# Optimization experiments

Hardware: AMD Instinct MI355X
Metric: run time of the kernel (lower is better)

## Reference

```python
import jax, jax.numpy as jnp
import numpy as np

B, L, C, H, DK, MAXREL = 4, 1024, 768, 12, 64, 7
NEG = -2.0 ** 15  # masked_fill value


def _rel_pos_table(L, m):
    # abs distance, compressed logarithmically beyond m, clipped to [0, 2m]
    i = jnp.arange(L, dtype=jnp.float32)
    d = jnp.abs(i[:, None] - i[None, :])
    comp = m + jnp.log2(jnp.maximum(d - m, 1.0))
    d = jnp.where(d > m, comp, d)
    return jnp.clip(d, 0, 2 * m).astype(jnp.int32)  # [L, L]


def setup_inputs() -> dict:
    key = jax.random.key(0)
    ks = jax.random.split(key, 16)
    s = 0.02
    return {
        "qx": jax.random.normal(ks[0], (B, L, C), jnp.float32),
        "kx": jax.random.normal(ks[1], (B, L, C), jnp.float32),
        "vx": jax.random.normal(ks[2], (B, L, C), jnp.float32),
        "WQ_w": jax.random.normal(ks[3], (C, H * DK), jnp.float32) * s,
        "WQ_b": jnp.zeros((H * DK,), jnp.float32),
        "WK_w": jax.random.normal(ks[4], (C, H * DK), jnp.float32) * s,
        "WK_b": jnp.zeros((H * DK,), jnp.float32),
        "WV_w": jax.random.normal(ks[5], (C, H * DK), jnp.float32) * s,
        "WV_b": jnp.zeros((H * DK,), jnp.float32),
        "WO_w": jax.random.normal(ks[6], (H * DK, C), jnp.float32) * s,
        "WO_b": jnp.zeros((C,), jnp.float32),
        "embK": jax.random.normal(ks[7], (2 * MAXREL + 1, H), jnp.float32),
        "embB": jax.random.normal(ks[8], (2 * MAXREL + 1, H), jnp.float32) * s,
        "preScores": jax.random.normal(ks[9], (B, H, L, L), jnp.float32) * 0.1,
        "maskPAD": jnp.ones((B, L, L), jnp.int32),
    }


def reference(qx, kx, vx, WQ_w, WQ_b, WK_w, WK_b, WV_w, WV_b, WO_w, WO_b,
              embK, embB, preScores, maskPAD):
    q = (qx @ WQ_w + WQ_b).reshape(B, L, H, DK).transpose(0, 2, 1, 3)  # [B,H,L,dk]
    k = (kx @ WK_w + WK_b).reshape(B, L, H, DK).transpose(0, 2, 1, 3)
    v = (vx @ WV_w + WV_b).reshape(B, L, H, DK).transpose(0, 2, 1, 3)

    scores = jnp.einsum('bhid,bhjd->bhij', q, k) / np.sqrt(DK).astype(np.float32)

    tab = _rel_pos_table(L, MAXREL)                 # [L, L] int
    relK = jnp.transpose(embK[tab], (2, 1, 0))      # [H, L, L] (torch transpose(0,-1))
    relB = jnp.transpose(embB[tab], (2, 1, 0))
    scores = scores * relK[None] + relB[None]

    scores = scores + preScores
    scores = jnp.where((maskPAD == 0)[:, None, :, :], jnp.float32(NEG), scores)

    alpha = jax.nn.softmax(scores, axis=-1)         # dropout is identity in eval
    z = jnp.einsum('bhij,bhjd->bhid', alpha, v)     # [B,H,L,dk]
    z = z.transpose(0, 2, 1, 3).reshape(B, L, H * DK)
    z = z @ WO_w + WO_b
    return (z, scores)
```

## Files before the change

kernel.cpp:

```cpp
#include <hip/hip_runtime.h>
#include <stdint.h>


typedef __attribute__((ext_vector_type(4))) float f32x4;
typedef __attribute__((ext_vector_type(4))) int   i32x4;
typedef __attribute__((ext_vector_type(8))) short short8;
typedef __attribute__((ext_vector_type(4))) unsigned int u32x4;
typedef __attribute__((ext_vector_type(2))) unsigned int u32x2;

__device__ __forceinline__ unsigned short f2bf(float f) {
  unsigned int u = __float_as_uint(f);
  u += 0x7fffu + ((u >> 16) & 1u);
  return (unsigned short)(u >> 16);
}

__global__ __launch_bounds__(256) void conv_x_kernel(
    const float* __restrict__ qx, const float* __restrict__ kx,
    const float* __restrict__ vx, unsigned short* __restrict__ out) {
  int v = blockIdx.x * 256 + threadIdx.x;
  int mat = v / 786432;
  int r = v - mat * 786432;
  const float* src = (mat == 0) ? qx : (mat == 1) ? kx : vx;
  f32x4 x = ((const f32x4*)src)[r];
  union { unsigned short s[4]; u32x2 u; } o;
  o.s[0] = f2bf(x[0]); o.s[1] = f2bf(x[1]); o.s[2] = f2bf(x[2]); o.s[3] = f2bf(x[3]);
  ((u32x2*)out)[v] = o.u;
}

__global__ __launch_bounds__(256) void conv_w_kernel(
    const float* __restrict__ w0, const float* __restrict__ w1,
    const float* __restrict__ w2, const float* __restrict__ w3,
    unsigned short* __restrict__ out) {
  __shared__ float T[64][65];
  int bx = blockIdx.x;
  int mat = bx / 144; int t2 = bx - mat * 144;
  int kt = t2 / 12, nt = t2 - kt * 12;
  int k0 = kt * 64, n0 = nt * 64;
  const float* W = (mat == 0) ? w0 : (mat == 1) ? w1 : (mat == 2) ? w2 : w3;
  unsigned short* WT = out + (size_t)mat * 589824;
  int t = threadIdx.x;
  int lr = t >> 4;
  int lc = (t & 15) * 4;
#pragma unroll
  for (int p = 0; p < 4; p++) {
    int row = p * 16 + lr;
    f32x4 x = *(const f32x4*)&W[(size_t)(k0 + row) * 768 + n0 + lc];
    T[lc + 0][row] = x[0]; T[lc + 1][row] = x[1];
    T[lc + 2][row] = x[2]; T[lc + 3][row] = x[3];
  }
  __syncthreads();
#pragma unroll
  for (int p = 0; p < 4; p++) {
    int row = p * 16 + lr;
    union { unsigned short s[4]; u32x2 u; } o;
    o.s[0] = f2bf(T[row][lc + 0]); o.s[1] = f2bf(T[row][lc + 1]);
    o.s[2] = f2bf(T[row][lc + 2]); o.s[3] = f2bf(T[row][lc + 3]);
    *(u32x2*)&WT[(size_t)(n0 + row) * 768 + k0 + lc] = o.u;
  }
}

__global__ __launch_bounds__(256, 2) void qkv_gemm_kernel(
    const unsigned short* __restrict__ xbf, const unsigned short* __restrict__ wt,
    const float* __restrict__ bq, const float* __restrict__ bk, const float* __restrict__ bv,
    unsigned short* __restrict__ qo, unsigned short* __restrict__ ko,
    unsigned short* __restrict__ vto) {
  __shared__ unsigned short SM[2][2][128 * 72];
  int bx = blockIdx.x;
  int mat = bx / 192; int rem = bx - mat * 192;
  int mt = rem / 6, nt = rem - mt * 6;
  int m0 = mt * 128, n0 = nt * 128;
  const unsigned short* A = xbf + (size_t)mat * 4096 * 768;
  const unsigned short* Bm = wt + (size_t)mat * 768 * 768;
  int t = threadIdx.x;
  int wave = t >> 6, lane = t & 63;
  int wm = (wave >> 1) * 64, wn = (wave & 1) * 64;
  int col = lane & 15, quad = lane >> 4;
  int srow = t >> 3;
  int sch = (t & 7) * 8;

  f32x4 acc[4][4];
#pragma unroll
  for (int i = 0; i < 4; i++)
#pragma unroll
    for (int j = 0; j < 4; j++) acc[i][j] = (f32x4){0.f, 0.f, 0.f, 0.f};

  u32x4 ra[4], rb[4];
#pragma unroll
  for (int p = 0; p < 4; p++) {
    ra[p] = *(const u32x4*)&A[(size_t)(m0 + srow + p * 32) * 768 + sch];
    rb[p] = *(const u32x4*)&Bm[(size_t)(n0 + srow + p * 32) * 768 + sch];
  }
#pragma unroll
  for (int p = 0; p < 4; p++) {
    *(u32x4*)&SM[0][0][(srow + p * 32) * 72 + sch] = ra[p];
    *(u32x4*)&SM[0][1][(srow + p * 32) * 72 + sch] = rb[p];
  }
#pragma unroll
  for (int p = 0; p < 4; p++) {
    ra[p] = *(const u32x4*)&A[(size_t)(m0 + srow + p * 32) * 768 + 64 + sch];
    rb[p] = *(const u32x4*)&Bm[(size_t)(n0 + srow + p * 32) * 768 + 64 + sch];
  }
  __syncthreads();

  for (int it = 0; it < 12; ++it) {
    const unsigned short* As = SM[it & 1][0];
    const unsigned short* Bs = SM[it & 1][1];
#pragma unroll
    for (int c = 0; c < 2; c++) {
      short8 af[4], bf[4];
#pragma unroll
      for (int i = 0; i < 4; i++) {
        af[i] = *(const short8*)&As[(wm + i * 16 + col) * 72 + c * 32 + quad * 8];
        bf[i] = *(const short8*)&Bs[(wn + i * 16 + col) * 72 + c * 32 + quad * 8];
      }
#pragma unroll
      for (int i = 0; i < 4; i++)
#pragma unroll
        for (int j = 0; j < 4; j++)
          acc[i][j] = __builtin_amdgcn_mfma_f32_16x16x32_bf16(af[i], bf[j], acc[i][j], 0, 0, 0);
    }
    if (it < 11) {
      unsigned short* An = SM[(it + 1) & 1][0];
      unsigned short* Bn = SM[(it + 1) & 1][1];
#pragma unroll
      for (int p = 0; p < 4; p++) {
        *(u32x4*)&An[(srow + p * 32) * 72 + sch] = ra[p];
        *(u32x4*)&Bn[(srow + p * 32) * 72 + sch] = rb[p];
      }
      if (it < 10) {
        int kk2 = (it + 2) * 64;
#pragma unroll
        for (int p = 0; p < 4; p++) {
          ra[p] = *(const u32x4*)&A[(size_t)(m0 + srow + p * 32) * 768 + kk2 + sch];
          rb[p] = *(const u32x4*)&Bm[(size_t)(n0 + srow + p * 32) * 768 + kk2 + sch];
        }
      }
      __syncthreads();
    }
  }

  if (mat != 2) {
    const float* bias = (mat == 0) ? bq : bk;
    unsigned short* dst = (mat == 0) ? qo : ko;
#pragma unroll
    for (int j = 0; j < 4; j++) {
      int gn = n0 + wn + j * 16 + col;
      float bsv = bias[gn];
      int h = gn >> 6, d = gn & 63;
#pragma unroll
      for (int i = 0; i < 4; i++) {
#pragma unroll
        for (int r = 0; r < 4; r++) {
          int gm = m0 + wm + i * 16 + quad * 4 + r;
          int b = gm >> 10, l = gm & 1023;
          dst[((size_t)(b * 12 + h) * 1024 + l) * 64 + d] = f2bf(acc[i][j][r] + bsv);
        }
      }
    }
  } else {
    unsigned short* Tr = &SM[0][0][0];
    __syncthreads();
#pragma unroll
    for (int j = 0; j < 4; j++) {
      int n = wn + j * 16 + col;
      float bsv = bv[n0 + n];
#pragma unroll
      for (int i = 0; i < 4; i++) {
        int m = wm + i * 16 + quad * 4;
        union { unsigned short s[4]; u32x2 u; } pk;
#pragma unroll
        for (int r = 0; r < 4; r++) pk.s[r] = f2bf(acc[i][j][r] + bsv);
        *(u32x2*)&Tr[(size_t)n * 132 + m] = pk.u;
      }
    }
    __syncthreads();
#pragma unroll
    for (int p = 0; p < 8; p++) {
      int row = (t >> 4) + p * 16;
      int ch = (t & 15) * 8;
      u32x4 val = *(const u32x4*)&Tr[(size_t)row * 132 + ch];
      int gn = n0 + row;
      int h = gn >> 6, d = gn & 63;
      int gm = m0 + ch;
      int b = gm >> 10, l = gm & 1023;
      *(u32x4*)&vto[((size_t)(b * 12 + h) * 64 + d) * 1024 + l] = val;
    }
  }
}

struct KV { u32x4 k0, k1, v0, v1; };

__device__ __forceinline__ void attn_body(
    int j0, int j2, bool stageNext, bool pf2,
    const unsigned short* KsC, const unsigned short* VsC,
    unsigned short* KsN, unsigned short* VsN,
    f32x4* preC, i32x4* mkC, KV& kvW, KV& kvF,
    const short8* qf, f32x4* oacc, float& m_s, float& l_s,
    const unsigned short* kbase, const unsigned short* vbase,
    const float* pbase, const int* mbase, float* sbase,
    unsigned short* Ps, const float* eK, const float* eB,
    int lrow, int gi, int srow, int sch, int col, int quad, int wave) {
  if (pf2) {
    kvF.k0 = *(const u32x4*)&kbase[(size_t)(j2 + srow) * 64 + sch];
    kvF.k1 = *(const u32x4*)&kbase[(size_t)(j2 + srow + 32) * 64 + sch];
    kvF.v0 = *(const u32x4*)&vbase[(size_t)srow * 1024 + j2 + sch];
    kvF.v1 = *(const u32x4*)&vbase[(size_t)(srow + 32) * 1024 + j2 + sch];
  }
  f32x4 sacc[4];
#pragma unroll
  for (int ns = 0; ns < 4; ns++) sacc[ns] = (f32x4){0.f, 0.f, 0.f, 0.f};
#pragma unroll
  for (int c = 0; c < 2; c++) {
#pragma unroll
    for (int ns = 0; ns < 4; ns++) {
      short8 kf = *(const short8*)&KsC[(ns * 16 + col) * 72 + c * 32 + quad * 8];
      sacc[ns] = __builtin_amdgcn_mfma_f32_16x16x32_bf16(kf, qf[c], sacc[ns], 0, 0, 0);
    }
  }
  float sv[4][4];
#pragma unroll
  for (int ns = 0; ns < 4; ns++) {
    int gj0 = j0 + ns * 16 + quad * 4;
    f32x4 sout;
#pragma unroll
    for (int r = 0; r < 4; r++) {
      int dd = gi - (gj0 + r); dd = dd < 0 ? -dd : dd;
      int idx;
      if (dd <= 7) idx = dd;
      else { idx = 38 - __clz(dd - 7); idx = idx > 14 ? 14 : idx; }
      float s = sacc[ns][r] * 0.125f * eK[idx] + eB[idx] + preC[ns][r];
      if (mkC[ns][r] == 0) s = -32768.0f;
      sout[r] = s; sv[ns][r] = s;
    }
    *(f32x4*)&sbase[(size_t)lrow * 1024 + gj0] = sout;
  }
  if (pf2) {
#pragma unroll
    for (int ns = 0; ns < 4; ns++) {
      preC[ns] = *(const f32x4*)&pbase[(size_t)lrow * 1024 + j2 + ns * 16 + quad * 4];
      mkC[ns] = *(const i32x4*)&mbase[(size_t)lrow * 1024 + j2 + ns * 16 + quad * 4];
    }
  }
  float mx = sv[0][0];
#pragma unroll
  for (int ns = 0; ns < 4; ns++)
#pragma unroll
    for (int r = 0; r < 4; r++) mx = fmaxf(mx, sv[ns][r]);
  mx = fmaxf(mx, __shfl_xor(mx, 16));
  mx = fmaxf(mx, __shfl_xor(mx, 32));
  float mn = fmaxf(m_s, mx);
  float alpha = __expf(m_s - mn);
  float rs = 0.f;
#pragma unroll
  for (int ns = 0; ns < 4; ns++)
#pragma unroll
    for (int r = 0; r < 4; r++) { float p = __expf(sv[ns][r] - mn); sv[ns][r] = p; rs += p; }
  rs += __shfl_xor(rs, 16); rs += __shfl_xor(rs, 32);
  l_s = l_s * alpha + rs;
  m_s = mn;
#pragma unroll
  for (int nd = 0; nd < 4; nd++)
#pragma unroll
    for (int r = 0; r < 4; r++) oacc[nd][r] *= alpha;
#pragma unroll
  for (int ns = 0; ns < 4; ns++) {
    union { unsigned short s[4]; u32x2 u; } pk;
#pragma unroll
    for (int r = 0; r < 4; r++) pk.s[r] = f2bf(sv[ns][r]);
    *(u32x2*)&Ps[(size_t)lrow * 72 + ns * 16 + quad * 4] = pk.u;
  }
#pragma unroll
  for (int c2 = 0; c2 < 2; c2++) {
    short8 pf = *(const short8*)&Ps[(wave * 16 + col) * 72 + c2 * 32 + quad * 8];
#pragma unroll
    for (int nd = 0; nd < 4; nd++) {
      short8 vf = *(const short8*)&VsC[(nd * 16 + col) * 72 + c2 * 32 + quad * 8];
      oacc[nd] = __builtin_amdgcn_mfma_f32_16x16x32_bf16(vf, pf, oacc[nd], 0, 0, 0);
    }
  }
  if (stageNext) {
    *(u32x4*)&KsN[srow * 72 + sch] = kvW.k0;
    *(u32x4*)&KsN[(srow + 32) * 72 + sch] = kvW.k1;
    *(u32x4*)&VsN[srow * 72 + sch] = kvW.v0;
    *(u32x4*)&VsN[(srow + 32) * 72 + sch] = kvW.v1;
    __syncthreads();
  }
}

__global__ __launch_bounds__(256, 3) void attn_kernel(
    const unsigned short* __restrict__ q, const unsigned short* __restrict__ k,
    const unsigned short* __restrict__ vt, const float* __restrict__ preS,
    const int* __restrict__ maskP, const float* __restrict__ embK,
    const float* __restrict__ embB, float* __restrict__ scores,
    unsigned short* __restrict__ zpre) {
  __shared__ unsigned short Qs[64 * 72];
  __shared__ unsigned short KsB[2][64 * 72];
  __shared__ unsigned short VsB[2][64 * 72];
  __shared__ float eKs[16], eBs[16];
  int bx = blockIdx.x;
  int slice = bx % 48, it = bx / 48;
  int b = slice / 12, h = slice - b * 12;
  int i0 = it * 64;
  int t = threadIdx.x, wave = t >> 6, lane = t & 63;
  int col = lane & 15, quad = lane >> 4;
  int srow = t >> 3, sch = (t & 7) * 8;

  if (t < 15) { eKs[t] = embK[t * 12 + h]; eBs[t] = embB[t * 12 + h]; }

  const unsigned short* qbase = q + ((size_t)(b * 12 + h) * 1024 + i0) * 64;
  const unsigned short* kbase = k + (size_t)(b * 12 + h) * 1024 * 64;
  const unsigned short* vbase = vt + (size_t)(b * 12 + h) * 64 * 1024;
  const float* pbase = preS + ((size_t)(b * 12 + h) * 1024 + i0) * 1024;
  const int* mbase = maskP + ((size_t)b * 1024 + i0) * 1024;
  float* sbase = scores + ((size_t)(b * 12 + h) * 1024 + i0) * 1024;
  int lrow = wave * 16 + col;
  int gi = i0 + lrow;

#pragma unroll
  for (int p = 0; p < 2; p++) {
    int row = srow + p * 32;
    *(u32x4*)&Qs[row * 72 + sch] = *(const u32x4*)&qbase[(size_t)row * 64 + sch];
  }
  __syncthreads();
  short8 qf[2];
  qf[0] = *(const short8*)&Qs[(wave * 16 + col) * 72 + quad * 8];
  qf[1] = *(const short8*)&Qs[(wave * 16 + col) * 72 + 32 + quad * 8];

  f32x4 oacc[4];
#pragma unroll
  for (int nd = 0; nd < 4; nd++) oacc[nd] = (f32x4){0.f, 0.f, 0.f, 0.f};
  float m_s = -3.0e38f, l_s = 0.f;

  int jt0 = it & 15;
  int t0 = jt0 * 64;
  int t1 = ((jt0 + 1) & 15) * 64;

  KV kvA, kvB;
  f32x4 preA[4], preB[4];
  i32x4 mkA[4], mkB[4];
  kvA.k0 = *(const u32x4*)&kbase[(size_t)(t0 + srow) * 64 + sch];
  kvA.k1 = *(const u32x4*)&kbase[(size_t)(t0 + srow + 32) * 64 + sch];
  kvA.v0 = *(const u32x4*)&vbase[(size_t)srow * 1024 + t0 + sch];
  kvA.v1 = *(const u32x4*)&vbase[(size_t)(srow + 32) * 1024 + t0 + sch];
  *(u32x4*)&KsB[0][srow * 72 + sch] = kvA.k0;
  *(u32x4*)&KsB[0][(srow + 32) * 72 + sch] = kvA.k1;
  *(u32x4*)&VsB[0][srow * 72 + sch] = kvA.v0;
  *(u32x4*)&VsB[0][(srow + 32) * 72 + sch] = kvA.v1;
#pragma unroll
  for (int ns = 0; ns < 4; ns++) {
    preA[ns] = *(const f32x4*)&pbase[(size_t)lrow * 1024 + t0 + ns * 16 + quad * 4];
    mkA[ns] = *(const i32x4*)&mbase[(size_t)lrow * 1024 + t0 + ns * 16 + quad * 4];
    preB[ns] = *(const f32x4*)&pbase[(size_t)lrow * 1024 + t1 + ns * 16 + quad * 4];
    mkB[ns] = *(const i32x4*)&mbase[(size_t)lrow * 1024 + t1 + ns * 16 + quad * 4];
  }
  kvB.k0 = *(const u32x4*)&kbase[(size_t)(t1 + srow) * 64 + sch];
  kvB.k1 = *(const u32x4*)&kbase[(size_t)(t1 + srow + 32) * 64 + sch];
  kvB.v0 = *(const u32x4*)&vbase[(size_t)srow * 1024 + t1 + sch];
  kvB.v1 = *(const u32x4*)&vbase[(size_t)(srow + 32) * 1024 + t1 + sch];
  __syncthreads();

  unsigned short* Ps = Qs;
  for (int n = 0; n < 16; n += 2) {
    int ja = ((jt0 + n) & 15) * 64;
    int jb = ((jt0 + n + 1) & 15) * 64;
    int jc = ((jt0 + n + 2) & 15) * 64;
    int jd = ((jt0 + n + 3) & 15) * 64;
    attn_body(ja, jc, n < 15, n < 14,
              KsB[0], VsB[0], KsB[1], VsB[1], preA, mkA, kvB, kvA,
              qf, oacc, m_s, l_s, kbase, vbase, pbase, mbase, sbase,
              Ps, eKs, eBs, lrow, gi, srow, sch, col, quad, wave);
    attn_body(jb, jd, n + 1 < 15, n + 1 < 14,
              KsB[1], VsB[1], KsB[0], VsB[0], preB, mkB, kvA, kvB,
              qf, oacc, m_s, l_s, kbase, vbase, pbase, mbase, sbase,
              Ps, eKs, eBs, lrow, gi, srow, sch, col, quad, wave);
  }

  float inv = 1.0f / fmaxf(l_s, 1e-30f);
  unsigned short* zb = zpre + ((size_t)(b * 12 + h) * 1024 + i0 + lrow) * 64;
#pragma unroll
  for (int nd = 0; nd < 4; nd++) {
    union { unsigned short s[4]; u32x2 u; } zk;
#pragma unroll
    for (int r = 0; r < 4; r++) zk.s[r] = f2bf(oacc[nd][r] * inv);
    *(u32x2*)&zb[nd * 16 + quad * 4] = zk.u;
  }
}

__global__ __launch_bounds__(256, 3) void out_gemm_kernel(
    const unsigned short* __restrict__ zpre, const unsigned short* __restrict__ wot,
    const float* __restrict__ wob, float* __restrict__ zout) {
  __shared__ unsigned short SM[2][2][64 * 72];
  int bx = blockIdx.x;
  int mt = bx / 12, nt = bx - mt * 12;
  int m0 = mt * 64, n0 = nt * 64;
  int t = threadIdx.x;
  int wave = t >> 6, lane = t & 63;
  int wm = (wave >> 1) * 32, wn = (wave & 1) * 32;
  int col = lane & 15, quad = lane >> 4;
  int srow = t >> 3, sch = (t & 7) * 8;
  int gmA0 = m0 + srow, gmA1 = m0 + srow + 32;
  int bA0 = gmA0 >> 10, lA0 = gmA0 & 1023;
  int bA1 = gmA1 >> 10, lA1 = gmA1 & 1023;

  f32x4 acc[2][2];
#pragma unroll
  for (int i = 0; i < 2; i++)
#pragma unroll
    for (int j = 0; j < 2; j++) acc[i][j] = (f32x4){0.f, 0.f, 0.f, 0.f};

  u32x4 ra[2], rb[2];
  ra[0] = *(const u32x4*)&zpre[((size_t)(bA0 * 12 + 0) * 1024 + lA0) * 64 + sch];
  ra[1] = *(const u32x4*)&zpre[((size_t)(bA1 * 12 + 0) * 1024 + lA1) * 64 + sch];
  rb[0] = *(const u32x4*)&wot[(size_t)(n0 + srow) * 768 + sch];
  rb[1] = *(const u32x4*)&wot[(size_t)(n0 + srow + 32) * 768 + sch];
  *(u32x4*)&SM[0][0][srow * 72 + sch] = ra[0];
  *(u32x4*)&SM[0][0][(srow + 32) * 72 + sch] = ra[1];
  *(u32x4*)&SM[0][1][srow * 72 + sch] = rb[0];
  *(u32x4*)&SM[0][1][(srow + 32) * 72 + sch] = rb[1];
  ra[0] = *(const u32x4*)&zpre[((size_t)(bA0 * 12 + 1) * 1024 + lA0) * 64 + sch];
  ra[1] = *(const u32x4*)&zpre[((size_t)(bA1 * 12 + 1) * 1024 + lA1) * 64 + sch];
  rb[0] = *(const u32x4*)&wot[(size_t)(n0 + srow) * 768 + 64 + sch];
  rb[1] = *(const u32x4*)&wot[(size_t)(n0 + srow + 32) * 768 + 64 + sch];
  __syncthreads();

  for (int it = 0; it < 12; ++it) {
    const unsigned short* As = SM[it & 1][0];
    const unsigned short* Bs = SM[it & 1][1];
#pragma unroll
    for (int c = 0; c < 2; c++) {
      short8 af[2], bf[2];
#pragma unroll
      for (int i = 0; i < 2; i++) {
        af[i] = *(const short8*)&As[(wm + i * 16 + col) * 72 + c * 32 + quad * 8];
        bf[i] = *(const short8*)&Bs[(wn + i * 16 + col) * 72 + c * 32 + quad * 8];
      }
#pragma unroll
      for (int i = 0; i < 2; i++)
#pragma unroll
        for (int j = 0; j < 2; j++)
          acc[i][j] = __builtin_amdgcn_mfma_f32_16x16x32_bf16(af[i], bf[j], acc[i][j], 0, 0, 0);
    }
    if (it < 11) {
      unsigned short* An = SM[(it + 1) & 1][0];
      unsigned short* Bn = SM[(it + 1) & 1][1];
      *(u32x4*)&An[srow * 72 + sch] = ra[0];
      *(u32x4*)&An[(srow + 32) * 72 + sch] = ra[1];
      *(u32x4*)&Bn[srow * 72 + sch] = rb[0];
      *(u32x4*)&Bn[(srow + 32) * 72 + sch] = rb[1];
      if (it < 10) {
        int hh = it + 2;
        ra[0] = *(const u32x4*)&zpre[((size_t)(bA0 * 12 + hh) * 1024 + lA0) * 64 + sch];
        ra[1] = *(const u32x4*)&zpre[((size_t)(bA1 * 12 + hh) * 1024 + lA1) * 64 + sch];
        rb[0] = *(const u32x4*)&wot[(size_t)(n0 + srow) * 768 + hh * 64 + sch];
        rb[1] = *(const u32x4*)&wot[(size_t)(n0 + srow + 32) * 768 + hh * 64 + sch];
      }
      __syncthreads();
    }
  }
#pragma unroll
  for (int j = 0; j < 2; j++) {
    int gn = n0 + wn + j * 16 + col;
    float bsv = wob[gn];
#pragma unroll
    for (int i = 0; i < 2; i++) {
#pragma unroll
      for (int r = 0; r < 4; r++) {
        int gm = m0 + wm + i * 16 + quad * 4 + r;
        zout[(size_t)gm * 768 + gn] = acc[i][j][r] + bsv;
      }
    }
  }
}

extern "C" void kernel_launch(void* const* d_in, const int* in_sizes, int n_in,
                              void* d_out, int out_size, void* d_ws, size_t ws_size,
                              hipStream_t stream) {
  const float* qx   = (const float*)d_in[0];
  const float* kx   = (const float*)d_in[1];
  const float* vx   = (const float*)d_in[2];
  const float* WQ_w = (const float*)d_in[3];
  const float* WQ_b = (const float*)d_in[4];
  const float* WK_w = (const float*)d_in[5];
  const float* WK_b = (const float*)d_in[6];
  const float* WV_w = (const float*)d_in[7];
  const float* WV_b = (const float*)d_in[8];
  const float* WO_w = (const float*)d_in[9];
  const float* WO_b = (const float*)d_in[10];
  const float* embK = (const float*)d_in[11];
  const float* embB = (const float*)d_in[12];
  const float* preS = (const float*)d_in[13];
  const int* maskP  = (const int*)d_in[14];

  float* zout = (float*)d_out;
  float* scores = zout + 3145728;
  unsigned short* xbf = (unsigned short*)scores;

  char* ws = (char*)d_ws;
  unsigned short* wt  = (unsigned short*)(ws);
  unsigned short* qb  = (unsigned short*)(ws + 4718592);
  unsigned short* kb  = (unsigned short*)(ws + 11010048);
  unsigned short* vtb = (unsigned short*)(ws + 17301504);
  unsigned short* zp  = (unsigned short*)(ws + 23592960);

  conv_x_kernel<<<9216, 256, 0, stream>>>(qx, kx, vx, xbf);
  conv_w_kernel<<<576, 256, 0, stream>>>(WQ_w, WK_w, WV_w, WO_w, wt);
  qkv_gemm_kernel<<<576, 256, 0, stream>>>(xbf, wt, WQ_b, WK_b, WV_b, qb, kb, vtb);
  attn_kernel<<<768, 256, 0, stream>>>(qb, kb, vtb, preS, maskP, embK, embB, scores, zp);
  out_gemm_kernel<<<192 * 4, 256, 0, stream>>>(zp, wt + 3 * 589824, WO_b, zout);
}
```

Before: 497.6 us.

## Pack padding mask into bitmask and load preScores in 256-column chunks

Adds a pre-pass that compresses the int32 padding mask into one bit per element, stored in the output buffer before the out-GEMM overwrites it. The attention kernel reads these bits instead of re-reading the full int32 mask for each of the 12 heads. The kernel also restructures its KV loop into four 256-column super-steps, prefetching 16 preScores vectors per step instead of two tiles of 4. This cuts redundant mask traffic but raises register pressure and adds an extra launch.

New measurement: 508.3 us. 1.02x slower.

```diff
diff --git a/kernel.cpp b/kernel.cpp
--- a/kernel.cpp
+++ b/kernel.cpp
@@ -25,6 +25,21 @@
   union { unsigned short s[4]; u32x2 u; } o;
   o.s[0] = f2bf(x[0]); o.s[1] = f2bf(x[1]); o.s[2] = f2bf(x[2]); o.s[3] = f2bf(x[3]);
   ((u32x2*)out)[v] = o.u;
+}
+
+__global__ __launch_bounds__(256) void conv_mask_kernel(
+    const int* __restrict__ m, unsigned int* __restrict__ out) {
+  int w = blockIdx.x * 256 + threadIdx.x;
+  const int* src = m + (size_t)w * 32;
+  unsigned int bits = 0u;
+#pragma unroll
+  for (int c = 0; c < 8; c++) {
+    i32x4 v = *(const i32x4*)&src[c * 4];
+#pragma unroll
+    for (int r = 0; r < 4; r++)
+      bits |= (v[r] != 0 ? 1u : 0u) << (c * 4 + r);
+  }
+  out[w] = bits;
 }
 
 __global__ __launch_bounds__(256) void conv_w_kernel(
@@ -190,107 +205,10 @@
 
 struct KV { u32x4 k0, k1, v0, v1; };
 
-__device__ __forceinline__ void attn_body(
-    int j0, int j2, bool stageNext, bool pf2,
-    const unsigned short* KsC, const unsigned short* VsC,
-    unsigned short* KsN, unsigned short* VsN,
-    f32x4* preC, i32x4* mkC, KV& kvW, KV& kvF,
-    const short8* qf, f32x4* oacc, float& m_s, float& l_s,
-    const unsigned short* kbase, const unsigned short* vbase,
-    const float* pbase, const int* mbase, float* sbase,
-    unsigned short* Ps, const float* eK, const float* eB,
-    int lrow, int gi, int srow, int sch, int col, int quad, int wave) {
-  if (pf2) {
-    kvF.k0 = *(const u32x4*)&kbase[(size_t)(j2 + srow) * 64 + sch];
-    kvF.k1 = *(const u32x4*)&kbase[(size_t)(j2 + srow + 32) * 64 + sch];
-    kvF.v0 = *(const u32x4*)&vbase[(size_t)srow * 1024 + j2 + sch];
-    kvF.v1 = *(const u32x4*)&vbase[(size_t)(srow + 32) * 1024 + j2 + sch];
-  }
-  f32x4 sacc[4];
-#pragma unroll
-  for (int ns = 0; ns < 4; ns++) sacc[ns] = (f32x4){0.f, 0.f, 0.f, 0.f};
-#pragma unroll
-  for (int c = 0; c < 2; c++) {
-#pragma unroll
-    for (int ns = 0; ns < 4; ns++) {
-      short8 kf = *(const short8*)&KsC[(ns * 16 + col) * 72 + c * 32 + quad * 8];
-      sacc[ns] = __builtin_amdgcn_mfma_f32_16x16x32_bf16(kf, qf[c], sacc[ns], 0, 0, 0);
-    }
-  }
-  float sv[4][4];
-#pragma unroll
-  for (int ns = 0; ns < 4; ns++) {
-    int gj0 = j0 + ns * 16 + quad * 4;
-    f32x4 sout;
-#pragma unroll
-    for (int r = 0; r < 4; r++) {
-      int dd = gi - (gj0 + r); dd = dd < 0 ? -dd : dd;
-      int idx;
-      if (dd <= 7) idx = dd;
-      else { idx = 38 - __clz(dd - 7); idx = idx > 14 ? 14 : idx; }
-      float s = sacc[ns][r] * 0.125f * eK[idx] + eB[idx] + preC[ns][r];
-      if (mkC[ns][r] == 0) s = -32768.0f;
-      sout[r] = s; sv[ns][r] = s;
-    }
-    *(f32x4*)&sbase[(size_t)lrow * 1024 + gj0] = sout;
-  }
-  if (pf2) {
-#pragma unroll
-    for (int ns = 0; ns < 4; ns++) {
-      preC[ns] = *(const f32x4*)&pbase[(size_t)lrow * 1024 + j2 + ns * 16 + quad * 4];
-      mkC[ns] = *(const i32x4*)&mbase[(size_t)lrow * 1024 + j2 + ns * 16 + quad * 4];
-    }
-  }
-  float mx = sv[0][0];
-#pragma unroll
-  for (int ns = 0; ns < 4; ns++)
-#pragma unroll
-    for (int r = 0; r < 4; r++) mx = fmaxf(mx, sv[ns][r]);
-  mx = fmaxf(mx, __shfl_xor(mx, 16));
-  mx = fmaxf(mx, __shfl_xor(mx, 32));
-  float mn = fmaxf(m_s, mx);
-  float alpha = __expf(m_s - mn);
-  float rs = 0.f;
-#pragma unroll
-  for (int ns = 0; ns < 4; ns++)
-#pragma unroll
-    for (int r = 0; r < 4; r++) { float p = __expf(sv[ns][r] - mn); sv[ns][r] = p; rs += p; }
-  rs += __shfl_xor(rs, 16); rs += __shfl_xor(rs, 32);
-  l_s = l_s * alpha + rs;
-  m_s = mn;
-#pragma unroll
-  for (int nd = 0; nd < 4; nd++)
-#pragma unroll
-    for (int r = 0; r < 4; r++) oacc[nd][r] *= alpha;
-#pragma unroll
-  for (int ns = 0; ns < 4; ns++) {
-    union { unsigned short s[4]; u32x2 u; } pk;
-#pragma unroll
-    for (int r = 0; r < 4; r++) pk.s[r] = f2bf(sv[ns][r]);
-    *(u32x2*)&Ps[(size_t)lrow * 72 + ns * 16 + quad * 4] = pk.u;
-  }
-#pragma unroll
-  for (int c2 = 0; c2 < 2; c2++) {
-    short8 pf = *(const short8*)&Ps[(wave * 16 + col) * 72 + c2 * 32 + quad * 8];
-#pragma unroll
-    for (int nd = 0; nd < 4; nd++) {
-      short8 vf = *(const short8*)&VsC[(nd * 16 + col) * 72 + c2 * 32 + quad * 8];
-      oacc[nd] = __builtin_amdgcn_mfma_f32_16x16x32_bf16(vf, pf, oacc[nd], 0, 0, 0);
-    }
-  }
-  if (stageNext) {
-    *(u32x4*)&KsN[srow * 72 + sch] = kvW.k0;
-    *(u32x4*)&KsN[(srow + 32) * 72 + sch] = kvW.k1;
-    *(u32x4*)&VsN[srow * 72 + sch] = kvW.v0;
-    *(u32x4*)&VsN[(srow + 32) * 72 + sch] = kvW.v1;
-    __syncthreads();
-  }
-}
-
 __global__ __launch_bounds__(256, 3) void attn_kernel(
     const unsigned short* __restrict__ q, const unsigned short* __restrict__ k,
     const unsigned short* __restrict__ vt, const float* __restrict__ preS,
-    const int* __restrict__ maskP, const float* __restrict__ embK,
+    const unsigned int* __restrict__ maskbits, const float* __restrict__ embK,
     const float* __restrict__ embB, float* __restrict__ scores,
     unsigned short* __restrict__ zpre) {
   __shared__ unsigned short Qs[64 * 72];
@@ -311,10 +229,12 @@
   const unsigned short* kbase = k + (size_t)(b * 12 + h) * 1024 * 64;
   const unsigned short* vbase = vt + (size_t)(b * 12 + h) * 64 * 1024;
   const float* pbase = preS + ((size_t)(b * 12 + h) * 1024 + i0) * 1024;
-  const int* mbase = maskP + ((size_t)b * 1024 + i0) * 1024;
   float* sbase = scores + ((size_t)(b * 12 + h) * 1024 + i0) * 1024;
   int lrow = wave * 16 + col;
   int gi = i0 + lrow;
+  const unsigned int* mrow = maskbits + ((size_t)(b * 1024 + i0 + lrow)) * 32;
+  const float* prow = pbase + (size_t)lrow * 1024;
+  float* srow_p = sbase + (size_t)lrow * 1024;
 
 #pragma unroll
   for (int p = 0; p < 2; p++) {
@@ -331,57 +251,148 @@
   for (int nd = 0; nd < 4; nd++) oacc[nd] = (f32x4){0.f, 0.f, 0.f, 0.f};
   float m_s = -3.0e38f, l_s = 0.f;
 
-  int jt0 = it & 15;
-  int t0 = jt0 * 64;
-  int t1 = ((jt0 + 1) & 15) * 64;
-
-  KV kvA, kvB;
-  f32x4 preA[4], preB[4];
-  i32x4 mkA[4], mkB[4];
-  kvA.k0 = *(const u32x4*)&kbase[(size_t)(t0 + srow) * 64 + sch];
-  kvA.k1 = *(const u32x4*)&kbase[(size_t)(t0 + srow + 32) * 64 + sch];
-  kvA.v0 = *(const u32x4*)&vbase[(size_t)srow * 1024 + t0 + sch];
-  kvA.v1 = *(const u32x4*)&vbase[(size_t)(srow + 32) * 1024 + t0 + sch];
-  *(u32x4*)&KsB[0][srow * 72 + sch] = kvA.k0;
-  *(u32x4*)&KsB[0][(srow + 32) * 72 + sch] = kvA.k1;
-  *(u32x4*)&VsB[0][srow * 72 + sch] = kvA.v0;
-  *(u32x4*)&VsB[0][(srow + 32) * 72 + sch] = kvA.v1;
-#pragma unroll
-  for (int ns = 0; ns < 4; ns++) {
-    preA[ns] = *(const f32x4*)&pbase[(size_t)lrow * 1024 + t0 + ns * 16 + quad * 4];
-    mkA[ns] = *(const i32x4*)&mbase[(size_t)lrow * 1024 + t0 + ns * 16 + quad * 4];
-    preB[ns] = *(const f32x4*)&pbase[(size_t)lrow * 1024 + t1 + ns * 16 + quad * 4];
-    mkB[ns] = *(const i32x4*)&mbase[(size_t)lrow * 1024 + t1 + ns * 16 + quad * 4];
-  }
-  kvB.k0 = *(const u32x4*)&kbase[(size_t)(t1 + srow) * 64 + sch];
-  kvB.k1 = *(const u32x4*)&kbase[(size_t)(t1 + srow + 32) * 64 + sch];
-  kvB.v0 = *(const u32x4*)&vbase[(size_t)srow * 1024 + t1 + sch];
-  kvB.v1 = *(const u32x4*)&vbase[(size_t)(srow + 32) * 1024 + t1 + sch];
+  int s0 = it & 3;
+
+  KV kv0, kv1;
+  int j0p = (s0 << 8);
+  int j1p = (s0 << 8) + 64;
+  kv0.k0 = *(const u32x4*)&kbase[(size_t)(j0p + srow) * 64 + sch];
+  kv0.k1 = *(const u32x4*)&kbase[(size_t)(j0p + srow + 32) * 64 + sch];
+  kv0.v0 = *(const u32x4*)&vbase[(size_t)srow * 1024 + j0p + sch];
+  kv0.v1 = *(const u32x4*)&vbase[(size_t)(srow + 32) * 1024 + j0p + sch];
+  *(u32x4*)&KsB[0][srow * 72 + sch] = kv0.k0;
+  *(u32x4*)&KsB[0][(srow + 32) * 72 + sch] = kv0.k1;
+  *(u32x4*)&VsB[0][srow * 72 + sch] = kv0.v0;
+  *(u32x4*)&VsB[0][(srow + 32) * 72 + sch] = kv0.v1;
+  kv1.k0 = *(const u32x4*)&kbase[(size_t)(j1p + srow) * 64 + sch];
+  kv1.k1 = *(const u32x4*)&kbase[(size_t)(j1p + srow + 32) * 64 + sch];
+  kv1.v0 = *(const u32x4*)&vbase[(size_t)srow * 1024 + j1p + sch];
+  kv1.v1 = *(const u32x4*)&vbase[(size_t)(srow + 32) * 1024 + j1p + sch];
+
+  f32x4 preC[16];
+#pragma unroll
+  for (int c = 0; c < 16; c++)
+    preC[c] = *(const f32x4*)&prow[(s0 << 8) + c * 16 + quad * 4];
+  u32x4 mw0 = *(const u32x4*)&mrow[(s0 << 3)];
+  u32x4 mw1 = *(const u32x4*)&mrow[(s0 << 3) + 4];
   __syncthreads();
 
   unsigned short* Ps = Qs;
-  for (int n = 0; n < 16; n += 2) {
-    int ja = ((jt0 + n) & 15) * 64;
-    int jb = ((jt0 + n + 1) & 15) * 64;
-    int jc = ((jt0 + n + 2) & 15) * 64;
-    int jd = ((jt0 + n + 3) & 15) * 64;
-    attn_body(ja, jc, n < 15, n < 14,
-              KsB[0], VsB[0], KsB[1], VsB[1], preA, mkA, kvB, kvA,
-              qf, oacc, m_s, l_s, kbase, vbase, pbase, mbase, sbase,
-              Ps, eKs, eBs, lrow, gi, srow, sch, col, quad, wave);
-    attn_body(jb, jd, n + 1 < 15, n + 1 < 14,
-              KsB[1], VsB[1], KsB[0], VsB[0], preB, mkB, kvA, kvB,
-              qf, oacc, m_s, l_s, kbase, vbase, pbase, mbase, sbase,
-              Ps, eKs, eBs, lrow, gi, srow, sch, col, quad, wave);
+
+  for (int s = 0; s < 4; ++s) {
+    int js = ((s0 + s) & 3) << 8;
+    int jsn = ((s0 + s + 1) & 3) << 8;
+#pragma unroll
+    for (int qq = 0; qq < 4; qq++) {
+      int j0 = js + (qq << 6);
+      bool fill = (s < 3) || (qq < 2);
+      bool stageNext = (s < 3) || (qq < 3);
+      const unsigned short* KsC = KsB[qq & 1];
+      const unsigned short* VsC = VsB[qq & 1];
+      unsigned short* KsN = KsB[(qq + 1) & 1];
+      unsigned short* VsN = VsB[(qq + 1) & 1];
+      KV& kvF = (qq & 1) ? kv1 : kv0;
+      KV& kvW = (qq & 1) ? kv0 : kv1;
+
+      if (fill) {
+        int j2 = (qq < 2) ? (js + ((qq + 2) << 6)) : (jsn + ((qq - 2) << 6));
+        kvF.k0 = *(const u32x4*)&kbase[(size_t)(j2 + srow) * 64 + sch];
+        kvF.k1 = *(const u32x4*)&kbase[(size_t)(j2 + srow + 32) * 64 + sch];
+        kvF.v0 = *(const u32x4*)&vbase[(size_t)srow * 1024 + j2 + sch];
+        kvF.v1 = *(const u32x4*)&vbase[(size_t)(srow + 32) * 1024 + j2 + sch];
+      }
+      f32x4 sacc[4];
+#pragma unroll
+      for (int ns = 0; ns < 4; ns++) sacc[ns] = (f32x4){0.f, 0.f, 0.f, 0.f};
+#pragma unroll
+      for (int c = 0; c < 2; c++) {
+#pragma unroll
+        for (int ns = 0; ns < 4; ns++) {
+          short8 kf = *(const short8*)&KsC[(ns * 16 + col) * 72 + c * 32 + quad * 8];
+          sacc[ns] = __builtin_amdgcn_mfma_f32_16x16x32_bf16(kf, qf[c], sacc[ns], 0, 0, 0);
+        }
+      }
+      float sv[4][4];
+#pragma unroll
+      for (int ns = 0; ns < 4; ns++) {
+        int gj0 = j0 + ns * 16 + quad * 4;
+        unsigned int wsel = (qq & 2) ? mw1[((qq & 1) << 1) + (ns >> 1)]
+                                     : mw0[((qq & 1) << 1) + (ns >> 1)];
+        unsigned int hb = (wsel >> (((ns & 1) << 4) + (quad << 2))) & 0xFu;
+        f32x4 sout;
+#pragma unroll
+        for (int r = 0; r < 4; r++) {
+          int dd = gi - (gj0 + r); dd = dd < 0 ? -dd : dd;
+          int idx;
+          if (dd <= 7) idx = dd;
+          else { idx = 38 - __clz(dd - 7); idx = idx > 14 ? 14 : idx; }
+          float sx = sacc[ns][r] * 0.125f * eKs[idx] + eBs[idx] + preC[qq * 4 + ns][r];
+          if (((hb >> r) & 1u) == 0u) sx = -32768.0f;
+          sout[r] = sx; sv[ns][r] = sx;
+        }
+        *(f32x4*)&srow_p[gj0] = sout;
+      }
+      if (qq == 3 && s < 3) {
+#pragma unroll
+        for (int c = 0; c < 16; c++)
+          preC[c] = *(const f32x4*)&prow[jsn + c * 16 + quad * 4];
+        mw0 = *(const u32x4*)&mrow[jsn >> 5];
+        mw1 = *(const u32x4*)&mrow[(jsn >> 5) + 4];
+      }
+      float mx = sv[0][0];
+#pragma unroll
+      for (int ns = 0; ns < 4; ns++)
+#pragma unroll
+        for (int r = 0; r < 4; r++) mx = fmaxf(mx, sv[ns][r]);
+      mx = fmaxf(mx, __shfl_xor(mx, 16));
+      mx = fmaxf(mx, __shfl_xor(mx, 32));
+      float mn = fmaxf(m_s, mx);
+      float alpha = __expf(m_s - mn);
+      float rs = 0.f;
+#pragma unroll
+      for (int ns = 0; ns < 4; ns++)
+#pragma unroll
+        for (int r = 0; r < 4; r++) { float p = __expf(sv[ns][r] - mn); sv[ns][r] = p; rs += p; }
+      rs += __shfl_xor(rs, 16); rs += __shfl_xor(rs, 32);
+      l_s = l_s * alpha + rs;
+      m_s = mn;
+#pragma unroll
+      for (int nd = 0; nd < 4; nd++)
+#pragma unroll
+        for (int r = 0; r < 4; r++) oacc[nd][r] *= alpha;
+#pragma unroll
+      for (int ns = 0; ns < 4; ns++) {
+        union { unsigned short sp[4]; u32x2 u; } pk;
+#pragma unroll
+        for (int r = 0; r < 4; r++) pk.sp[r] = f2bf(sv[ns][r]);
+        *(u32x2*)&Ps[(size_t)lrow * 72 + ns * 16 + quad * 4] = pk.u;
+      }
+#pragma unroll
+      for (int c2 = 0; c2 < 2; c2++) {
+        short8 pf = *(const short8*)&Ps[(wave * 16 + col) * 72 + c2 * 32 + quad * 8];
+#pragma unroll
+        for (int nd = 0; nd < 4; nd++) {
+          short8 vf = *(const short8*)&VsC[(nd * 16 + col) * 72 + c2 * 32 + quad * 8];
+          oacc[nd] = __builtin_amdgcn_mfma_f32_16x16x32_bf16(vf, pf, oacc[nd], 0, 0, 0);
+        }
+      }
+      if (stageNext) {
+        *(u32x4*)&KsN[srow * 72 + sch] = kvW.k0;
+        *(u32x4*)&KsN[(srow + 32) * 72 + sch] = kvW.k1;
+        *(u32x4*)&VsN[srow * 72 + sch] = kvW.v0;
+        *(u32x4*)&VsN[(srow + 32) * 72 + sch] = kvW.v1;
+        __syncthreads();
+      }
+    }
   }
 
   float inv = 1.0f / fmaxf(l_s, 1e-30f);
   unsigned short* zb = zpre + ((size_t)(b * 12 + h) * 1024 + i0 + lrow) * 64;
 #pragma unroll
   for (int nd = 0; nd < 4; nd++) {
-    union { unsigned short s[4]; u32x2 u; } zk;
-#pragma unroll
-    for (int r = 0; r < 4; r++) zk.s[r] = f2bf(oacc[nd][r] * inv);
+    union { unsigned short sp[4]; u32x2 u; } zk;
+#pragma unroll
+    for (int r = 0; r < 4; r++) zk.sp[r] = f2bf(oacc[nd][r] * inv);
     *(u32x2*)&zb[nd * 16 + quad * 4] = zk.u;
   }
 }
@@ -494,6 +505,7 @@
   float* zout = (float*)d_out;
   float* scores = zout + 3145728;
   unsigned short* xbf = (unsigned short*)scores;
+  unsigned int* mbits = (unsigned int*)zout;
 
   char* ws = (char*)d_ws;
   unsigned short* wt  = (unsigned short*)(ws);
@@ -503,8 +515,9 @@
   unsigned short* zp  = (unsigned short*)(ws + 23592960);
 
   conv_x_kernel<<<9216, 256, 0, stream>>>(qx, kx, vx, xbf);
+  conv_mask_kernel<<<512, 256, 0, stream>>>(maskP, mbits);
   conv_w_kernel<<<576, 256, 0, stream>>>(WQ_w, WK_w, WV_w, WO_w, wt);
   qkv_gemm_kernel<<<576, 256, 0, stream>>>(xbf, wt, WQ_b, WK_b, WV_b, qb, kb, vtb);
-  attn_kernel<<<768, 256, 0, stream>>>(qb, kb, vtb, preS, maskP, embK, embB, scores, zp);
+  attn_kernel<<<768, 256, 0, stream>>>(qb, kb, vtb, preS, mbits, embK, embB, scores, zp);
   out_gemm_kernel<<<192 * 4, 256, 0, stream>>>(zp, wt + 3 * 589824, WO_b, zout);
 }
```
